# Kernel optimization log

Measured on AMD Instinct MI355X. Metric: run time of the kernel, lower is better.

The kernel has to match this reference:

```python
import jax, jax.numpy as jnp
import numpy as np

D_MODEL = 1024
N_HEADS = 16
HEAD_DIM = D_MODEL // N_HEADS
D_FF = 4 * D_MODEL
SEQ = 2048
BATCH = 2
EPS = 1e-6


def setup_inputs() -> dict:
    key = jax.random.key(0)
    ks = jax.random.split(key, 8)
    s = 0.02
    return {
        "x": jax.random.normal(ks[0], (SEQ, BATCH, D_MODEL), dtype=jnp.float32),
        "g1": jnp.ones((D_MODEL,), dtype=jnp.float32),                # norm1 weight
        "g2": jnp.ones((D_MODEL,), dtype=jnp.float32),                # norm2 weight
        "Wq": jax.random.normal(ks[1], (N_HEADS, D_MODEL, HEAD_DIM), dtype=jnp.float32) * s,
        "Wk": jax.random.normal(ks[2], (N_HEADS, D_MODEL, HEAD_DIM), dtype=jnp.float32) * s,
        "Wv": jax.random.normal(ks[3], (N_HEADS, D_MODEL, HEAD_DIM), dtype=jnp.float32) * s,
        "Wo": jax.random.normal(ks[4], (D_MODEL, D_MODEL), dtype=jnp.float32) * s,
        "W1": jax.random.normal(ks[5], (D_MODEL, D_FF), dtype=jnp.float32) * s,
        "W2": jax.random.normal(ks[6], (D_FF, D_MODEL), dtype=jnp.float32) * s,
    }


def _rmsnorm(x, g):
    rms = jnp.sqrt(jnp.mean(x * x, axis=-1, keepdims=True) + EPS)
    return g * (x / rms)


def _block(x, g1, g2, Wq, Wk, Wv, Wo, W1, W2):
    S = x.shape[0]
    scale = HEAD_DIM ** -0.5
    # --- attention (pre-norm) ---
    h = _rmsnorm(x, g1)                              # (S, B, D)
    Q = jnp.einsum('sbd,hdk->bhsk', h, Wq)           # (B, H, S, K)
    K = jnp.einsum('sbd,hdk->bhsk', h, Wk)
    V = jnp.einsum('sbd,hdk->bhsk', h, Wv)
    scores = jnp.einsum('bhsk,bhtk->bhst', Q, K) * scale
    causal = jnp.tril(jnp.ones((S, S), dtype=bool))
    scores = jnp.where(causal, scores, -jnp.inf)
    attn = jax.nn.softmax(scores, axis=-1)
    ctx = jnp.einsum('bhst,bhtk->sbhk', attn, V)     # heads concatenated in order
    ctx = ctx.reshape(S, x.shape[1], D_MODEL)
    x = x + ctx @ Wo
    # --- FFN (pre-norm) ---
    h2 = _rmsnorm(x, g2)
    x = x + jax.nn.silu(h2 @ W1) @ W2
    return x


def reference(x, g1, g2, Wq, Wk, Wv, Wo, W1, W2):
    return _block(x, g1, g2, Wq, Wk, Wv, Wo, W1, W2)
```

## Files before the change

### kernel.cpp

```cpp
#include <hip/hip_runtime.h>

typedef unsigned short u16;
typedef __bf16 bf16x8 __attribute__((ext_vector_type(8)));
typedef u16 u16x8 __attribute__((ext_vector_type(8)));
typedef u16 u16x4 __attribute__((ext_vector_type(4)));
typedef float f32x4 __attribute__((ext_vector_type(4)));

__device__ __forceinline__ u16 f2bf(float f) {
    union { float f; unsigned int u; } x; x.f = f;
    unsigned int r = x.u + 0x7FFFu + ((x.u >> 16) & 1u);
    return (u16)(r >> 16);
}

__device__ __forceinline__ void gload_lds16(const u16* g, u16* l) {
    __builtin_amdgcn_global_load_lds(
        (const __attribute__((address_space(1))) unsigned int*)g,
        (__attribute__((address_space(3))) unsigned int*)l, 16, 0, 0);
}


__global__ __launch_bounds__(256) void qkvT_k(
    const float* __restrict__ Wq, const float* __restrict__ Wk,
    const float* __restrict__ Wv, u16* __restrict__ out)
{
    __shared__ float T[64][65];
    const int d0 = blockIdx.x * 64;
    const int y = blockIdx.y;
    const int wsel = y >> 4, h = y & 15;
    const float* W = (wsel == 0) ? Wq : (wsel == 1) ? Wk : Wv;
    const float scale = (wsel == 0) ? 0.125f * 1.44269504088896f : 1.0f;
    const int tid = threadIdx.x;
    const int tr = tid >> 4;
    const int tc = (tid & 15) * 4;
    #pragma unroll
    for (int k = 0; k < 4; k++) {
        f32x4 v = *(const f32x4*)(W + (size_t)h * 65536 + (size_t)(d0 + 16 * k + tr) * 64 + tc);
        T[16 * k + tr][tc]     = v[0];
        T[16 * k + tr][tc + 1] = v[1];
        T[16 * k + tr][tc + 2] = v[2];
        T[16 * k + tr][tc + 3] = v[3];
    }
    __syncthreads();
    #pragma unroll
    for (int k = 0; k < 4; k++) {
        const int kk = 16 * k + tr;
        u16x4 o;
        #pragma unroll
        for (int i = 0; i < 4; i++) o[i] = f2bf(T[tc + i][kk] * scale);
        *(u16x4*)(out + (size_t)(wsel * 1024 + h * 64 + kk) * 1024 + d0 + tc) = o;
    }
}

__global__ __launch_bounds__(256) void transT_k(
    const float* __restrict__ in, u16* __restrict__ out, int R, int C)
{
    __shared__ float T[64][65];
    const int r0 = blockIdx.x * 64, c0 = blockIdx.y * 64;
    const int tid = threadIdx.x;
    const int tr = tid >> 4;
    const int tc = (tid & 15) * 4;
    #pragma unroll
    for (int k = 0; k < 4; k++) {
        f32x4 v = *(const f32x4*)(in + (size_t)(c0 + 16 * k + tr) * R + r0 + tc);
        T[16 * k + tr][tc]     = v[0];
        T[16 * k + tr][tc + 1] = v[1];
        T[16 * k + tr][tc + 2] = v[2];
        T[16 * k + tr][tc + 3] = v[3];
    }
    __syncthreads();
    #pragma unroll
    for (int k = 0; k < 4; k++) {
        const int rl = 16 * k + tr;
        u16x4 o;
        #pragma unroll
        for (int i = 0; i < 4; i++) o[i] = f2bf(T[tc + i][rl]);
        *(u16x4*)(out + (size_t)(r0 + rl) * C + c0 + tc) = o;
    }
}

__global__ __launch_bounds__(256) void vtrans_k(const u16* __restrict__ qkv, u16* __restrict__ vT)
{
    __shared__ u16 T[64][72];
    const int bh = blockIdx.x, b = bh >> 4, h = bh & 15;
    const int s0 = blockIdx.y * 64;
    const int tid = threadIdx.x;
    const int r = tid >> 2, c0 = (tid & 3) * 16;
    const u16* src = qkv + ((size_t)((s0 + r) * 2 + b)) * 3072 + 2048 + h * 64 + c0;
    *(u16x8*)&T[r][c0] = *(const u16x8*)src;
    *(u16x8*)&T[r][c0 + 8] = *(const u16x8*)(src + 8);
    __syncthreads();
    u16x8 o0, o1;
    #pragma unroll
    for (int i = 0; i < 8; i++) o0[i] = T[c0 + i][r];
    #pragma unroll
    for (int i = 0; i < 8; i++) o1[i] = T[c0 + 8 + i][r];
    u16* dst = vT + (size_t)(bh * 64 + r) * 2048 + s0 + c0;
    *(u16x8*)dst = o0;
    *(u16x8*)(dst + 8) = o1;
}

__global__ __launch_bounds__(256) void rmsnorm_k(
    const float* __restrict__ x, const float* __restrict__ g, u16* __restrict__ out)
{
    const int row = blockIdx.x;
    const int tid = threadIdx.x;
    const float* xr = x + (size_t)row * 1024;
    f32x4 v = *(const f32x4*)(xr + tid * 4);
    float ss = v[0] * v[0] + v[1] * v[1] + v[2] * v[2] + v[3] * v[3];
    #pragma unroll
    for (int off = 32; off > 0; off >>= 1) ss += __shfl_down(ss, off);
    __shared__ float red[4];
    if ((tid & 63) == 0) red[tid >> 6] = ss;
    __syncthreads();
    float sum = red[0] + red[1] + red[2] + red[3];
    float rinv = rsqrtf(sum * (1.0f / 1024.0f) + 1e-6f);
    f32x4 gv = *(const f32x4*)(g + tid * 4);
    u16x4 o;
    #pragma unroll
    for (int i = 0; i < 4; i++) o[i] = f2bf(v[i] * gv[i] * rinv);
    *(u16x4*)(out + (size_t)row * 1024 + tid * 4) = o;
}

__global__ __launch_bounds__(256) void addred_norm_k(
    const float* __restrict__ res, const float* __restrict__ p0,
    const float* __restrict__ p1, const float* __restrict__ g,
    float* __restrict__ xout, u16* __restrict__ hout)
{
    const int row = blockIdx.x;
    const int tid = threadIdx.x;
    const size_t base = (size_t)row * 1024 + tid * 4;
    f32x4 a = *(const f32x4*)(res + base);
    f32x4 b = *(const f32x4*)(p0 + base);
    f32x4 c = *(const f32x4*)(p1 + base);
    f32x4 o = a + b + c;
    *(f32x4*)(xout + base) = o;
    float ss = o[0] * o[0] + o[1] * o[1] + o[2] * o[2] + o[3] * o[3];
    #pragma unroll
    for (int off = 32; off > 0; off >>= 1) ss += __shfl_down(ss, off);
    __shared__ float red[4];
    if ((tid & 63) == 0) red[tid >> 6] = ss;
    __syncthreads();
    float sum = red[0] + red[1] + red[2] + red[3];
    float rinv = rsqrtf(sum * (1.0f / 1024.0f) + 1e-6f);
    f32x4 gv = *(const f32x4*)(g + tid * 4);
    u16x4 hv;
    #pragma unroll
    for (int i = 0; i < 4; i++) hv[i] = f2bf(o[i] * gv[i] * rinv);
    *(u16x4*)(hout + base) = hv;
}

__global__ __launch_bounds__(256) void addred_k(
    const float* __restrict__ res, const float* __restrict__ p0,
    const float* __restrict__ p1, float* __restrict__ out)
{
    int i = (blockIdx.x * 256 + threadIdx.x) * 4;
    f32x4 a = *(const f32x4*)(res + i);
    f32x4 b = *(const f32x4*)(p0 + i);
    f32x4 c = *(const f32x4*)(p1 + i);
    f32x4 o = a + b + c;
    *(f32x4*)(out + i) = o;
}

template <int MODE>
__global__ __launch_bounds__(256) void gemm_bt_k(
    const u16* __restrict__ A, const u16* __restrict__ BT,
    u16* __restrict__ outB, float* __restrict__ outF, const float* __restrict__ res,
    int M, int N, int K, int klen)
{
    __shared__ u16 As[128][32];
    __shared__ u16 Bs[128][32];
    const int tid = threadIdx.x;
    const int lane = tid & 63, w = tid >> 6;
    const int wm = w >> 1, wn = w & 1;
    const int quad = lane >> 4, l15 = lane & 15;
    const int bid = blockIdx.x + gridDim.x * blockIdx.y;
    const int bj = bid >> 3;
    const int m0 = ((bid & 7) * 4 + (bj & 3)) * 128;
    const int n0 = (bj >> 2) * 128;
    const int kbeg = blockIdx.z * klen;

    f32x4 acc[4][4] = {};

    const int srow = w * 16 + (lane >> 2);
    const int scol = (lane & 3) * 8;
    const u16* aA0 = A + (size_t)(m0 + srow) * K + kbeg + scol;
    const u16* aA1 = A + (size_t)(m0 + 64 + srow) * K + kbeg + scol;
    const u16* aB0 = BT + (size_t)(n0 + srow) * K + kbeg + scol;
    const u16* aB1 = BT + (size_t)(n0 + 64 + srow) * K + kbeg + scol;
    u16* ldsA0 = &As[0][0] + w * 512;
    u16* ldsA1 = &As[0][0] + 2048 + w * 512;
    u16* ldsB0 = &Bs[0][0] + w * 512;
    u16* ldsB1 = &Bs[0][0] + 2048 + w * 512;

    for (int k0 = 0; k0 < klen; k0 += 32) {
        __syncthreads();
        gload_lds16(aA0 + k0, ldsA0);
        gload_lds16(aA1 + k0, ldsA1);
        gload_lds16(aB0 + k0, ldsB0);
        gload_lds16(aB1 + k0, ldsB1);
        __syncthreads();
        bf16x8 af[4], bfr[4];
        #pragma unroll
        for (int i = 0; i < 4; i++) af[i] = *(const bf16x8*)&As[wm * 64 + i * 16 + l15][quad * 8];
        #pragma unroll
        for (int j = 0; j < 4; j++) bfr[j] = *(const bf16x8*)&Bs[wn * 64 + j * 16 + l15][quad * 8];
        #pragma unroll
        for (int i = 0; i < 4; i++)
            #pragma unroll
            for (int j = 0; j < 4; j++)
                acc[i][j] = __builtin_amdgcn_mfma_f32_16x16x32_bf16(af[i], bfr[j], acc[i][j], 0, 0, 0);
    }

    float* outFz = (MODE == 3) ? outF + (size_t)blockIdx.z * M * N : outF;
    #pragma unroll
    for (int i = 0; i < 4; i++) {
        const int row = m0 + wm * 64 + i * 16 + quad * 4;
        #pragma unroll
        for (int j = 0; j < 4; j++) {
            const int col = n0 + wn * 64 + j * 16 + l15;
            #pragma unroll
            for (int r = 0; r < 4; r++) {
                const size_t idx = (size_t)(row + r) * N + col;
                float v = acc[i][j][r];
                if (MODE == 0) {
                    outB[idx] = f2bf(v);
                } else if (MODE == 1) {
                    outF[idx] = res[idx] + v;
                } else if (MODE == 2) {
                    outB[idx] = f2bf(v / (1.0f + __expf(-v)));
                } else {
                    outFz[idx] = v;
                }
            }
        }
    }
}

__global__ __launch_bounds__(256) void attn_k(const u16* __restrict__ qkv,
                                              const u16* __restrict__ vT,
                                              u16* __restrict__ ctx)
{
    const int bh = blockIdx.x;
    const int qt = 31 - (int)blockIdx.y;
    const int b = bh >> 4, h = bh & 15;
    const int q0 = qt * 64;
    const int tid = threadIdx.x;
    const int lane = tid & 63, w = tid >> 6;
    const int quad = lane >> 4, l15 = lane & 15;

    __shared__ u16 QP[64][72];
    __shared__ u16 Ks[2][4096];
    __shared__ u16 Vs[2][4096];

    {
        const int r = tid >> 2, c0 = (tid & 3) * 16;
        const u16* src = qkv + ((size_t)((q0 + r) * 2 + b)) * 3072 + h * 64 + c0;
        *(u16x8*)&QP[r][c0] = *(const u16x8*)(src);
        *(u16x8*)&QP[r][c0 + 8] = *(const u16x8*)(src + 8);
    }
    __syncthreads();

    const bf16x8 aq0 = *(const bf16x8*)&QP[16 * w + l15][quad * 8];
    const bf16x8 aq1 = *(const bf16x8*)&QP[16 * w + l15][32 + quad * 8];

    const int kr = (w << 3) + (lane >> 3);
    const int swz = ((lane & 7) ^ (lane >> 3)) << 3;
    const int ldsoff = w * 512;
    const u16* kbase0 = qkv + ((size_t)(kr * 2 + b)) * 3072 + 1024 + h * 64 + swz;
    const u16* kbase1 = kbase0 + (size_t)32 * 2 * 3072;
    const u16* vrow0 = vT + (size_t)(bh * 64 + kr) * 2048 + swz;
    const u16* vrow1 = vrow0 + (size_t)32 * 2048;

    const int rsw = (l15 & 7) << 3;

    f32x4 o[4] = {};
    float l4[4] = { 0.f, 0.f, 0.f, 0.f };

    gload_lds16(kbase0, &Ks[0][0] + ldsoff);
    gload_lds16(kbase1, &Ks[0][0] + 2048 + ldsoff);
    gload_lds16(vrow0, &Vs[0][0] + ldsoff);
    gload_lds16(vrow1, &Vs[0][0] + 2048 + ldsoff);

    int cur = 0;
    for (int t0 = 0; t0 <= q0; t0 += 64) {
        __syncthreads();
        if (t0 + 64 <= q0) {
            const size_t go = (size_t)(t0 + 64) * 2 * 3072;
            u16* KB = &Ks[cur ^ 1][0];
            u16* VB = &Vs[cur ^ 1][0];
            gload_lds16(kbase0 + go, KB + ldsoff);
            gload_lds16(kbase1 + go, KB + 2048 + ldsoff);
            gload_lds16(vrow0 + (t0 + 64), VB + ldsoff);
            gload_lds16(vrow1 + (t0 + 64), VB + 2048 + ldsoff);
        }
        const u16* KB = &Ks[cur][0];
        const u16* VB = &Vs[cur][0];

        f32x4 s[4];
        #pragma unroll
        for (int j = 0; j < 4; j++) {
            const u16* kb = KB + (j * 16 + l15) * 64;
            bf16x8 bk0 = *(const bf16x8*)(kb + (((quad << 3) ^ rsw)));
            bf16x8 bk1 = *(const bf16x8*)(kb + ((((quad + 4) << 3) ^ rsw)));
            f32x4 c = {};
            c = __builtin_amdgcn_mfma_f32_16x16x32_bf16(aq0, bk0, c, 0, 0, 0);
            c = __builtin_amdgcn_mfma_f32_16x16x32_bf16(aq1, bk1, c, 0, 0, 0);
            s[j] = c;
        }

        if (t0 == q0) {
            #pragma unroll
            for (int j = 0; j < 4; j++)
                #pragma unroll
                for (int r = 0; r < 4; r++)
                    if ((j * 16 + l15) > (16 * w + quad * 4 + r)) s[j][r] = -1e30f;
        }

        float rs[4] = { 0.f, 0.f, 0.f, 0.f };
        #pragma unroll
        for (int j = 0; j < 4; j++)
            #pragma unroll
            for (int r = 0; r < 4; r++) {
                float p = exp2f(s[j][r]);
                s[j][r] = p;
                rs[r] += p;
            }
        #pragma unroll
        for (int r = 0; r < 4; r++) {
            float t = rs[r];
            t += __shfl_xor(t, 1);
            t += __shfl_xor(t, 2);
            t += __shfl_xor(t, 4);
            t += __shfl_xor(t, 8);
            l4[r] += t;
        }

        #pragma unroll
        for (int j = 0; j < 4; j++)
            #pragma unroll
            for (int r = 0; r < 4; r++)
                QP[16 * w + quad * 4 + r][j * 16 + l15] = f2bf(s[j][r]);

        bf16x8 ap0 = *(const bf16x8*)&QP[16 * w + l15][quad * 8];
        bf16x8 ap1 = *(const bf16x8*)&QP[16 * w + l15][32 + quad * 8];
        #pragma unroll
        for (int j = 0; j < 4; j++) {
            const u16* vb = VB + (j * 16 + l15) * 64;
            bf16x8 bv0 = *(const bf16x8*)(vb + (((quad << 3) ^ rsw)));
            bf16x8 bv1 = *(const bf16x8*)(vb + ((((quad + 4) << 3) ^ rsw)));
            o[j] = __builtin_amdgcn_mfma_f32_16x16x32_bf16(ap0, bv0, o[j], 0, 0, 0);
            o[j] = __builtin_amdgcn_mfma_f32_16x16x32_bf16(ap1, bv1, o[j], 0, 0, 0);
        }
        cur ^= 1;
    }

    #pragma unroll
    for (int r = 0; r < 4; r++) l4[r] = 1.0f / l4[r];
    #pragma unroll
    for (int j = 0; j < 4; j++)
        #pragma unroll
        for (int r = 0; r < 4; r++) {
            int q = q0 + 16 * w + quad * 4 + r;
            int col = h * 64 + j * 16 + l15;
            ctx[((size_t)q * 2 + b) * 1024 + col] = f2bf(o[j][r] * l4[r]);
        }
}

extern "C" void kernel_launch(void* const* d_in, const int* in_sizes, int n_in,
                              void* d_out, int out_size, void* d_ws, size_t ws_size,
                              hipStream_t stream)
{
    (void)in_sizes; (void)n_in; (void)out_size; (void)ws_size;
    const float* x  = (const float*)d_in[0];
    const float* g1 = (const float*)d_in[1];
    const float* g2 = (const float*)d_in[2];
    const float* Wq = (const float*)d_in[3];
    const float* Wk = (const float*)d_in[4];
    const float* Wv = (const float*)d_in[5];
    const float* Wo = (const float*)d_in[6];
    const float* W1 = (const float*)d_in[7];
    const float* W2 = (const float*)d_in[8];
    float* out = (float*)d_out;

    char* ws = (char*)d_ws;
    u16*   bqkvT = (u16*)(ws);
    u16*   woT   = (u16*)(ws + 6291456);
    u16*   w1T   = (u16*)(ws + 8388608);
    u16*   w2T   = (u16*)(ws + 16777216);
    u16*   h1    = (u16*)(ws + 25165824);
    u16*   qkvB  = (u16*)(ws + 33554432);
    u16*   ctxB  = (u16*)(ws + 58720256);
    float* xmid  = (float*)(ws + 67108864);
    u16*   h2    = (u16*)(ws + 83886080);
    u16*   actB  = (u16*)(ws + 92274688);
    u16*   vT    = (u16*)(ws + 25165824);
    float* part  = (float*)(ws + 25165824);
    float* partO = (float*)(ws + 92274688);

    qkvT_k<<<dim3(16, 48), 256, 0, stream>>>(Wq, Wk, Wv, bqkvT);
    transT_k<<<dim3(16, 16), 256, 0, stream>>>(Wo, woT, 1024, 1024);
    transT_k<<<dim3(64, 16), 256, 0, stream>>>(W1, w1T, 4096, 1024);
    transT_k<<<dim3(16, 64), 256, 0, stream>>>(W2, w2T, 1024, 4096);

    rmsnorm_k<<<4096, 256, 0, stream>>>(x, g1, h1);

    gemm_bt_k<0><<<dim3(24, 32), 256, 0, stream>>>(h1, bqkvT, qkvB, nullptr, nullptr,
                                                   4096, 3072, 1024, 1024);
    vtrans_k<<<dim3(32, 32), 256, 0, stream>>>(qkvB, vT);
    attn_k<<<dim3(32, 32), 256, 0, stream>>>(qkvB, vT, ctxB);

    gemm_bt_k<3><<<dim3(8, 32, 2), 256, 0, stream>>>(ctxB, woT, nullptr, partO, nullptr,
                                                     4096, 1024, 1024, 512);
    addred_norm_k<<<4096, 256, 0, stream>>>(x, partO, partO + 4096 * 1024, g2, xmid, h2);

    gemm_bt_k<2><<<dim3(32, 32), 256, 0, stream>>>(h2, w1T, actB, nullptr, nullptr,
                                                   4096, 4096, 1024, 1024);
    gemm_bt_k<3><<<dim3(8, 32, 2), 256, 0, stream>>>(actB, w2T, nullptr, part, nullptr,
                                                     4096, 1024, 4096, 2048);
    addred_k<<<4096 * 1024 / 1024, 256, 0, stream>>>(xmid, part, part + 4096 * 1024, out);
}
```

Before: 374.4 us.

## Double GEMM K-tile to 64 with XOR-swizzled LDS layout

Each main-loop iteration of the bf16 GEMM now stages a 64-wide K slice instead of 32, which halves the number of barrier pairs per K pass. The LDS tiles get an XOR swizzle on the 16-byte column chunk, applied both when global_load_lds writes them and when the fragments are read back. The swizzle is meant to avoid the LDS bank conflicts that row-strided fragment reads would hit with 128-byte rows. In exchange, LDS use per block doubles to 32 KB, which may reduce occupancy. klen must also now be a multiple of 64.

```diff
diff --git a/kernel.cpp b/kernel.cpp
--- a/kernel.cpp
+++ b/kernel.cpp
@@ -167,8 +167,8 @@
     u16* __restrict__ outB, float* __restrict__ outF, const float* __restrict__ res,
     int M, int N, int K, int klen)
 {
-    __shared__ u16 As[128][32];
-    __shared__ u16 Bs[128][32];
+    __shared__ u16 As[128 * 64];
+    __shared__ u16 Bs[128 * 64];
     const int tid = threadIdx.x;
     const int lane = tid & 63, w = tid >> 6;
     const int wm = w >> 1, wn = w & 1;
@@ -181,34 +181,39 @@
 
     f32x4 acc[4][4] = {};
 
-    const int srow = w * 16 + (lane >> 2);
-    const int scol = (lane & 3) * 8;
-    const u16* aA0 = A + (size_t)(m0 + srow) * K + kbeg + scol;
-    const u16* aA1 = A + (size_t)(m0 + 64 + srow) * K + kbeg + scol;
-    const u16* aB0 = BT + (size_t)(n0 + srow) * K + kbeg + scol;
-    const u16* aB1 = BT + (size_t)(n0 + 64 + srow) * K + kbeg + scol;
-    u16* ldsA0 = &As[0][0] + w * 512;
-    u16* ldsA1 = &As[0][0] + 2048 + w * 512;
-    u16* ldsB0 = &Bs[0][0] + w * 512;
-    u16* ldsB1 = &Bs[0][0] + 2048 + w * 512;
-
-    for (int k0 = 0; k0 < klen; k0 += 32) {
+    const int srow = (w << 3) + (lane >> 3);
+    const int swz = ((lane & 7) ^ (lane >> 3)) << 3;
+    const u16* aA = A + (size_t)(m0 + srow) * K + kbeg + swz;
+    const u16* aB = BT + (size_t)(n0 + srow) * K + kbeg + swz;
+    u16* lA = As + w * 512;
+    u16* lB = Bs + w * 512;
+    const int rsw = (l15 & 7) << 3;
+
+    for (int k0 = 0; k0 < klen; k0 += 64) {
         __syncthreads();
-        gload_lds16(aA0 + k0, ldsA0);
-        gload_lds16(aA1 + k0, ldsA1);
-        gload_lds16(aB0 + k0, ldsB0);
-        gload_lds16(aB1 + k0, ldsB1);
+        #pragma unroll
+        for (int c = 0; c < 4; c++)
+            gload_lds16(aA + (size_t)(c * 32) * K + k0, lA + c * 2048);
+        #pragma unroll
+        for (int c = 0; c < 4; c++)
+            gload_lds16(aB + (size_t)(c * 32) * K + k0, lB + c * 2048);
         __syncthreads();
-        bf16x8 af[4], bfr[4];
-        #pragma unroll
-        for (int i = 0; i < 4; i++) af[i] = *(const bf16x8*)&As[wm * 64 + i * 16 + l15][quad * 8];
-        #pragma unroll
-        for (int j = 0; j < 4; j++) bfr[j] = *(const bf16x8*)&Bs[wn * 64 + j * 16 + l15][quad * 8];
-        #pragma unroll
-        for (int i = 0; i < 4; i++)
+        #pragma unroll
+        for (int kh = 0; kh < 2; kh++) {
+            const int cb = ((kh * 4 + quad) << 3);
+            bf16x8 af[4], bfr[4];
+            #pragma unroll
+            for (int i = 0; i < 4; i++)
+                af[i] = *(const bf16x8*)(As + (wm * 64 + i * 16 + l15) * 64 + (cb ^ rsw));
             #pragma unroll
             for (int j = 0; j < 4; j++)
-                acc[i][j] = __builtin_amdgcn_mfma_f32_16x16x32_bf16(af[i], bfr[j], acc[i][j], 0, 0, 0);
+                bfr[j] = *(const bf16x8*)(Bs + (wn * 64 + j * 16 + l15) * 64 + (cb ^ rsw));
+            #pragma unroll
+            for (int i = 0; i < 4; i++)
+                #pragma unroll
+                for (int j = 0; j < 4; j++)
+                    acc[i][j] = __builtin_amdgcn_mfma_f32_16x16x32_bf16(af[i], bfr[j], acc[i][j], 0, 0, 0);
+        }
     }
 
     float* outFz = (MODE == 3) ? outF + (size_t)blockIdx.z * M * N : outF;
```

Result: faster. 350.3 us (-6.4%).
